# Optimization experiments

Hardware: AMD Instinct MI355X
Metric: run time of the kernel (lower is better)

## Reference

```python
import jax, jax.numpy as jnp
import numpy as np
from jax import lax

ANGRES = 5


def _conv(x, w, stride=(1, 1), pad=((1, 1), (1, 1)), dil=(1, 1)):
    return lax.conv_general_dilated(x, w, stride, pad, rhs_dilation=dil,
                                    dimension_numbers=('NCHW', 'OIHW', 'NCHW'))


def _lrelu(x):
    return jnp.where(x >= 0, x, 0.1 * x)


def _block_s(x, w):
    # SAI input: split into 5x5 grid of (sh,sw) views, conv each view, emit MacPI-interleaved layout
    B, C, H, W = x.shape
    sh, sw = H // 5, W // 5
    p = x.reshape(B, C, 5, sh, 5, sw).transpose(0, 2, 4, 1, 3, 5).reshape(B * 25, C, sh, sw)
    y = _conv(p, w).reshape(B, 5, 5, C, sh, sw)
    # (B,bi,bj,C,sh,sw) -> (B,C,sh,bi,sw,bj) -> (B,C,H,W)   [torch permute(0,3,4,1,5,2)]
    return y.transpose(0, 3, 4, 1, 5, 2).reshape(B, C, H, W)


def _block_a(x, w):
    # MacPI input: conv each 5x5 macropixel independently (zero pad at block edges)
    B, C, H, W = x.shape
    nh, nw = H // 5, W // 5
    p = x.reshape(B, C, nh, 5, nw, 5).transpose(0, 2, 4, 1, 3, 5).reshape(B * nh * nw, C, 5, 5)
    y = _conv(p, w)
    return y.reshape(B, nh, nw, C, 5, 5).transpose(0, 3, 1, 4, 2, 5).reshape(B, C, H, W)


def _epi(x, w1, w2, a):
    # EPI conv: [1,3a] kernel, stride [1,a], pad [0,a]; then 1x1 to a*C; then 1D pixel shuffle on W
    y = _lrelu(_conv(x, w1, stride=(1, a), pad=((0, 0), (a, a))))
    y = _lrelu(_conv(y, w2, pad=((0, 0), (0, 0))))
    B, aC, H, Wa = y.shape
    C = aC // a
    return y.reshape(B, a, C, H, Wa).transpose(0, 2, 3, 4, 1).reshape(B, C, H, Wa * a)


def _att_fuse(buf, alpha, gamma, beta, eps=1e-5):
    # covariance-based GLU attention over the N=4 branches
    B, NC, H, W = buf.shape
    N = 4
    C = NC // N
    x5 = buf.reshape(B, N, C, H, W)
    xr = x5.reshape(B, N, C * H * W)
    M = xr.shape[-1]
    xc = xr - jnp.mean(xr, axis=-1, keepdims=True)
    cov = jnp.einsum('bnm,bkm->bnk', xc, xc) * (alpha / (M - 1))  # [B,N,N]
    norm = cov / jnp.sqrt(jnp.mean(cov * cov, axis=(1, 2), keepdims=True) + eps)
    g = gamma * norm + beta
    att = g * jax.nn.sigmoid(g)  # GLU of duplicated halves
    out = jnp.einsum('bnk,bkm->bnm', att, xr).reshape(B, N, C, H, W) + x5
    return out.reshape(B, NC, H, W)


def _mac2sai(x, a):
    B, C, HU, WV = x.shape
    h, w = HU // a, WV // a
    return x.reshape(B, C, a, h, a, w).transpose(0, 1, 3, 5, 2, 4).reshape(B, C, h * a, w * a)


def _tsfefb(x, x1, ws, wa, we1, we2, al, ga, be, wf1, wf2, a):
    feaSpa = _lrelu(_block_s(x1, ws))
    feaAng = _lrelu(_block_a(x, wa))
    feaH = _epi(x, we1, we2, a)
    feaV = jnp.transpose(_epi(jnp.transpose(x, (0, 1, 3, 2)), we1, we2, a), (0, 1, 3, 2))
    buf = jnp.concatenate([feaSpa, feaAng, feaH, feaV], axis=1)
    out = _att_fuse(buf, al, ga, be)
    y = _lrelu(_conv(out, wf1, pad=((0, 0), (0, 0))))
    y = _conv(y, wf2, pad=((a, a), (a, a)), dil=(a, a))
    return y + x


def setup_inputs() -> dict:
    key = jax.random.key(0)
    ks = jax.random.split(key, 12)
    B, C, a, n = 4, 64, ANGRES, 4
    H = W = a * 32  # 160

    def w(k, shape):
        fan_in = float(np.prod(shape[2:]))
        return jax.random.normal(k, shape, jnp.float32) / np.float32(np.sqrt(fan_in))

    return {
        'x': jax.random.normal(ks[0], (B, C, H, W), jnp.float32),
        'x1': jax.random.normal(ks[1], (B, C, H, W), jnp.float32),
        'w_spa': w(ks[2], (n, C, C, 3, 3)),
        'w_ang': w(ks[3], (n, C, C, 3, 3)),
        'w_epi1': w(ks[4], (n, C, C, 1, 3 * a)),
        'w_epi2': w(ks[5], (n, a * C, C, 1, 1)),
        'alpha': jnp.ones((n,), jnp.float32),
        'gamma': 0.1 * jax.random.normal(ks[6], (n,), jnp.float32),
        'beta': 0.1 * jax.random.normal(ks[7], (n,), jnp.float32),
        'w_fuse1': w(ks[8], (n, C, 4 * C, 1, 1)),
        'w_fuse2': w(ks[9], (n, C, C, 3, 3)),
    }


def reference(x, x1, w_spa, w_ang, w_epi1, w_epi2, alpha, gamma, beta, w_fuse1, w_fuse2):
    a = ANGRES
    buf, buf1 = x, x1
    for i in range(w_spa.shape[0]):
        buf = _tsfefb(buf, buf1, w_spa[i], w_ang[i], w_epi1[i], w_epi2[i],
                      alpha[i], gamma[i], beta[i], w_fuse1[i], w_fuse2[i], a)
        buf1 = _mac2sai(buf, a)
    return buf
```

## Files before the change

kernel.cpp:

```cpp
#include <hip/hip_runtime.h>

__device__ __forceinline__ float lrelu(float v){ return v >= 0.f ? v : 0.1f*v; }


__global__ __launch_bounds__(256) void k_spa(const float* __restrict__ buf1, const float* __restrict__ w,
                                             float* __restrict__ out){
  const int b = blockIdx.x / 50, r2 = blockIdx.x % 50;
  const int view = r2 >> 1, half = r2 & 1;
  const int bi = view / 5, bj = view % 5;
  const int th0 = half*16;
  const int cog = blockIdx.y;
  const int tid = threadIdx.x;
  __shared__ float plane[2][18*38];
  for (int idx=tid; idx<2*18*38; idx+=256) ((float*)plane)[idx]=0.f;
  float acc[2][8];
  #pragma unroll
  for (int k=0;k<2;k++)
    #pragma unroll
    for (int c=0;c<8;c++) acc[k][c]=0.f;
  const float* src = buf1 + (size_t)b*1638400 + bi*32*160 + bj*32;
  const float* wb = w + (size_t)(cog*8)*576;
  const int sr = tid >> 3, sq = (tid & 7)*4;
  const int vr = th0 - 1 + sr;
  const bool rowok = (tid < 144) && ((unsigned)vr < 32u);
  __syncthreads();
  if (rowok)
    *(float4*)&plane[0][sr*38 + 4 + sq] = *(const float4*)(src + vr*160 + sq);
  __syncthreads();
  const int lr = tid >> 5, c = tid & 31;
  for (int ci=0; ci<64; ci++){
    float4 nx;
    const bool ld = rowok && (ci < 63);
    if (ld) nx = *(const float4*)(src + (size_t)(ci+1)*25600 + vr*160 + sq);
    const float* P = plane[ci & 1];
    float t0[9], t1[9];
    {
      const float* pp = &P[lr*38 + c + 3];
      t0[0]=pp[0];  t0[1]=pp[1];  t0[2]=pp[2];
      t0[3]=pp[38]; t0[4]=pp[39]; t0[5]=pp[40];
      t0[6]=pp[76]; t0[7]=pp[77]; t0[8]=pp[78];
      const float* qq = pp + 8*38;
      t1[0]=qq[0];  t1[1]=qq[1];  t1[2]=qq[2];
      t1[3]=qq[38]; t1[4]=qq[39]; t1[5]=qq[40];
      t1[6]=qq[76]; t1[7]=qq[77]; t1[8]=qq[78];
    }
    #pragma unroll
    for (int co=0;co<8;co++){
      const float* wp = wb + (size_t)co*576 + ci*9;
      float w0=wp[0],w1=wp[1],w2=wp[2],w3=wp[3],w4=wp[4],w5=wp[5],w6=wp[6],w7=wp[7],w8=wp[8];
      acc[0][co] += t0[0]*w0+t0[1]*w1+t0[2]*w2+t0[3]*w3+t0[4]*w4
                  + t0[5]*w5+t0[6]*w6+t0[7]*w7+t0[8]*w8;
      acc[1][co] += t1[0]*w0+t1[1]*w1+t1[2]*w2+t1[3]*w3+t1[4]*w4
                  + t1[5]*w5+t1[6]*w6+t1[7]*w7+t1[8]*w8;
    }
    if (ld) *(float4*)&plane[(ci+1)&1][sr*38 + 4 + sq] = nx;
    __syncthreads();
  }
  #pragma unroll
  for (int k=0;k<2;k++){
    int si = th0 + lr + k*8;
    int h = si*5 + bi, wq = c*5 + bj;
    #pragma unroll
    for (int co=0;co<8;co++){
      int ch = b*64 + cog*8 + co;
      out[(size_t)ch*25600 + h*160 + wq] = lrelu(acc[k][co]);
    }
  }
}

__global__ __launch_bounds__(256) void k_ang(const float* __restrict__ bufA, const float* __restrict__ w,
                                             float* __restrict__ out){
  const int b = blockIdx.x >> 5, mi = blockIdx.x & 31;
  const int cog = blockIdx.y;
  const int tid = threadIdx.x;
  __shared__ float rowp[7*172];
  for (int idx=tid; idx<7*172; idx+=256) rowp[idx]=0.f;
  float acc[4][8];
  #pragma unroll
  for (int k=0;k<4;k++)
    #pragma unroll
    for (int c=0;c<8;c++) acc[k][c]=0.f;
  int pu[4], pbase[4];
  float plm[4], prm[4];
  bool act[4];
  #pragma unroll
  for (int k=0;k<4;k++){
    int p = tid + k*256;
    act[k] = p < 800;
    int pp = act[k] ? p : 0;
    int mp = pp/25; int pos = pp - mp*25;
    int u = pos/5, v = pos - u*5;
    pu[k] = u; pbase[k] = 4 + mp*5 + v - 1;
    plm[k] = (v!=0) ? 1.f : 0.f;
    prm[k] = (v!=4) ? 1.f : 0.f;
  }
  const float* src = bufA + (size_t)b*1638400 + mi*800;
  const float* wb = w + (size_t)(cog*8)*576;
  const int sr = tid/40, sq = (tid%40)*4;
  for (int ci=0; ci<64; ci++){
    __syncthreads();
    if (tid < 200)
      *(float4*)&rowp[(1+sr)*172 + 4 + sq] = *(const float4*)(src + (size_t)ci*25600 + sr*160 + sq);
    __syncthreads();
    float t[4][9];
    #pragma unroll
    for (int k=0;k<4;k++){
      if (act[k]){
        const float* pp = &rowp[pu[k]*172 + pbase[k]];
        float lm=plm[k], rm=prm[k];
        t[k][0]=pp[0]*lm;   t[k][1]=pp[1];   t[k][2]=pp[2]*rm;
        t[k][3]=pp[172]*lm; t[k][4]=pp[173]; t[k][5]=pp[174]*rm;
        t[k][6]=pp[344]*lm; t[k][7]=pp[345]; t[k][8]=pp[346]*rm;
      } else {
        #pragma unroll
        for (int j=0;j<9;j++) t[k][j]=0.f;
      }
    }
    #pragma unroll
    for (int c=0;c<8;c++){
      const float* wp = wb + (size_t)c*576 + ci*9;
      float w0=wp[0],w1=wp[1],w2=wp[2],w3=wp[3],w4=wp[4],w5=wp[5],w6=wp[6],w7=wp[7],w8=wp[8];
      #pragma unroll
      for (int k=0;k<4;k++)
        acc[k][c] += t[k][0]*w0+t[k][1]*w1+t[k][2]*w2+t[k][3]*w3+t[k][4]*w4
                   + t[k][5]*w5+t[k][6]*w6+t[k][7]*w7+t[k][8]*w8;
    }
  }
  #pragma unroll
  for (int k=0;k<4;k++){
    if (act[k]){
      int p = tid + k*256;
      int mp = p/25; int pos = p - mp*25;
      int u = pos/5, v = pos - u*5;
      int h = mi*5 + u, wq = mp*5 + v;
      #pragma unroll
      for (int c=0;c<8;c++){
        int ch = b*64 + cog*8 + c;
        out[(size_t)ch*25600 + h*160 + wq] = lrelu(acc[k][c]);
      }
    }
  }
}

template<int VERT>
__global__ __launch_bounds__(320) void k_epi(const float* __restrict__ bufA, const float* __restrict__ we1,
                                             const float* __restrict__ we2, float* __restrict__ out){
  const int b = blockIdx.x / 160, hw = blockIdx.x % 160;
  const int tid = threadIdx.x;
  __shared__ float rowp[64*176];
  __shared__ float y1s[64*32];
  if (VERT){
    for (int idx=tid; idx<10240; idx+=320){
      int ci = idx/160, x = idx - ci*160;
      rowp[ci*176 + 8 + x] = bufA[(size_t)b*1638400 + (size_t)ci*25600 + (size_t)x*160 + hw];
    }
  } else {
    for (int ft=tid; ft<2560; ft+=320){
      int ci = ft/40, xq = (ft - ci*40)*4;
      *(float4*)&rowp[ci*176 + 8 + xq] =
        *(const float4*)(bufA + (size_t)b*1638400 + (size_t)ci*25600 + (size_t)hw*160 + xq);
    }
  }
  for (int idx=tid; idx<64*16; idx+=320){
    int ci = idx>>4, j = idx&15;
    rowp[ci*176 + (j<8 ? j : 160+j)] = 0.f;
  }
  __syncthreads();
  if (tid < 256){
    const int co = tid >> 2, wv0 = (tid & 3)*8;
    const int a0 = 2 + wv0*5;
    float acc[8];
    #pragma unroll
    for (int j=0;j<8;j++) acc[j]=0.f;
    const float* wp0 = we1 + (size_t)co*960;
    for (int ci=0; ci<64; ci++){
      float fl[52];
      const float* rp = &rowp[ci*176 + a0];
      #pragma unroll
      for (int m=0;m<26;m++) *(float2*)&fl[2*m] = *(const float2*)&rp[2*m];
      const float* wp = wp0 + ci*15;
      #pragma unroll
      for (int t=0;t<15;t++){
        float wt = wp[t];
        #pragma unroll
        for (int j=0;j<8;j++) acc[j] += fl[1 + j*5 + t]*wt;
      }
    }
    #pragma unroll
    for (int j=0;j<8;j++) y1s[co*32 + wv0 + j] = lrelu(acc[j]);
  }
  __syncthreads();
  {
    const int oc = tid, kk = oc >> 6, c = oc & 63;
    float a2[32];
    #pragma unroll
    for (int wv=0;wv<32;wv++) a2[wv]=0.f;
    const float* wp = we2 + (size_t)oc*64;
    for (int ci=0; ci<64; ci++){
      float wt = wp[ci];
      const float* yp = &y1s[ci*32];
      #pragma unroll
      for (int wv=0; wv<32; wv++) a2[wv] += yp[wv]*wt;
    }
    float* y2s = rowp;
    #pragma unroll
    for (int wv=0; wv<32; wv++) y2s[c*160 + wv*5 + kk] = lrelu(a2[wv]);
  }
  __syncthreads();
  {
    const float* y2s = rowp;
    for (int k=0;k<8;k++){
      int f = (tid + k*320)*4;
      int c = f/160, rr = f - c*160;
      *(float4*)(out + (size_t)(b*64+c)*25600 + (size_t)hw*160 + rr) = *(const float4*)&y2s[c*160+rr];
    }
  }
}

__global__ __launch_bounds__(256) void k_permV(const float* __restrict__ tmp, float* __restrict__ dst){
  const int bc = blockIdx.x;
  const int ti = blockIdx.y / 5, tj = blockIdx.y % 5;
  const int hw0 = ti*32, r0 = tj*32;
  const int lx = threadIdx.x & 31, ly = threadIdx.x >> 5;
  __shared__ float tile[32][33];
  const float* in = tmp + (size_t)bc*25600;
  float* outp = dst + (size_t)bc*25600;
  for (int yy=ly; yy<32; yy+=8)
    tile[yy][lx] = in[(size_t)(hw0+yy)*160 + r0 + lx];
  __syncthreads();
  for (int yy=ly; yy<32; yy+=8)
    outp[(size_t)(r0+yy)*160 + hw0 + lx] = tile[lx][yy];
}

__global__ __launch_bounds__(256) void k_permM(const float* __restrict__ A, float* __restrict__ dst){
  const int bc = blockIdx.x >> 5, hh = blockIdx.x & 31;
  const int tid = threadIdx.x;
  __shared__ float rows[5*160];
  const float* in = A + (size_t)bc*25600;
  if (tid < 200){
    int ai = tid/40, q = (tid - ai*40)*4;
    *(float4*)&rows[ai*160 + q] = *(const float4*)(in + (size_t)(ai*32+hh)*160 + q);
  }
  __syncthreads();
  float* outp = dst + (size_t)bc*25600 + (size_t)hh*800;
  for (int t=tid; t<800; t+=256){
    int ww = t/25, r2 = t - ww*25, ai = r2/5, aj = r2 - ai*5;
    outp[t] = rows[ai*160 + aj*32 + ww];
  }
}

__global__ __launch_bounds__(256) void k_red(const float* __restrict__ b0, const float* __restrict__ b1,
                                             const float* __restrict__ b2, const float* __restrict__ b3,
                                             float* __restrict__ part){
  const int b = blockIdx.y, blk = blockIdx.x;
  const int tid = threadIdx.x;
  const size_t off = (size_t)b*1638400 + (size_t)blk*25600;
  float s0=0,s1=0,s2=0,s3=0;
  float p00=0,p01=0,p02=0,p03=0,p11=0,p12=0,p13=0,p22=0,p23=0,p33=0;
  for (int it=0; it<25; it++){
    size_t m = off + it*1024 + tid*4;
    float4 x0 = *(const float4*)(b0+m);
    float4 x1 = *(const float4*)(b1+m);
    float4 x2 = *(const float4*)(b2+m);
    float4 x3 = *(const float4*)(b3+m);
    s0 += (x0.x+x0.y)+(x0.z+x0.w);
    s1 += (x1.x+x1.y)+(x1.z+x1.w);
    s2 += (x2.x+x2.y)+(x2.z+x2.w);
    s3 += (x3.x+x3.y)+(x3.z+x3.w);
    p00 += x0.x*x0.x+x0.y*x0.y+x0.z*x0.z+x0.w*x0.w;
    p01 += x0.x*x1.x+x0.y*x1.y+x0.z*x1.z+x0.w*x1.w;
    p02 += x0.x*x2.x+x0.y*x2.y+x0.z*x2.z+x0.w*x2.w;
    p03 += x0.x*x3.x+x0.y*x3.y+x0.z*x3.z+x0.w*x3.w;
    p11 += x1.x*x1.x+x1.y*x1.y+x1.z*x1.z+x1.w*x1.w;
    p12 += x1.x*x2.x+x1.y*x2.y+x1.z*x2.z+x1.w*x2.w;
    p13 += x1.x*x3.x+x1.y*x3.y+x1.z*x3.z+x1.w*x3.w;
    p22 += x2.x*x2.x+x2.y*x2.y+x2.z*x2.z+x2.w*x2.w;
    p23 += x2.x*x3.x+x2.y*x3.y+x2.z*x3.z+x2.w*x3.w;
    p33 += x3.x*x3.x+x3.y*x3.y+x3.z*x3.z+x3.w*x3.w;
  }
  float vals[14] = {s0,s1,s2,s3,p00,p01,p02,p03,p11,p12,p13,p22,p23,p33};
  __shared__ float red[4][14];
  int lane = tid & 63, wv = tid >> 6;
  #pragma unroll
  for (int j=0;j<14;j++){
    float v = vals[j];
    #pragma unroll
    for (int o=32;o>0;o>>=1) v += __shfl_down(v,o,64);
    if (lane==0) red[wv][j]=v;
  }
  __syncthreads();
  if (tid<14) part[((size_t)b*64+blk)*16 + tid] = red[0][tid]+red[1][tid]+red[2][tid]+red[3][tid];
}

__global__ __launch_bounds__(256) void k_attW(const float* __restrict__ part,
        const float* __restrict__ alpha, const float* __restrict__ gamma, const float* __restrict__ beta,
        int iblk, const float* __restrict__ wf1, float* __restrict__ Weff){
  const int b = blockIdx.x, tid = threadIdx.x;
  __shared__ float st[14];
  __shared__ float att[16];
  if (tid<14){
    float t=0;
    for (int blk=0;blk<64;blk++) t += part[((size_t)b*64+blk)*16 + tid];
    st[tid]=t;
  }
  __syncthreads();
  if (tid==0){
    const float M = 1638400.f;
    float s[4] = {st[0],st[1],st[2],st[3]};
    float S[4][4];
    S[0][0]=st[4];  S[0][1]=S[1][0]=st[5];  S[0][2]=S[2][0]=st[6];  S[0][3]=S[3][0]=st[7];
    S[1][1]=st[8];  S[1][2]=S[2][1]=st[9];  S[1][3]=S[3][1]=st[10];
    S[2][2]=st[11]; S[2][3]=S[3][2]=st[12]; S[3][3]=st[13];
    float al=alpha[iblk], ga=gamma[iblk], be=beta[iblk];
    float scale = al/(M-1.f);
    float cov[4][4], ss=0.f;
    for (int n=0;n<4;n++) for (int k=0;k<4;k++){
      float c = (S[n][k] - s[n]*s[k]/M)*scale;
      cov[n][k]=c; ss += c*c;
    }
    float rms = sqrtf(ss/16.f + 1e-5f);
    for (int n=0;n<4;n++) for (int k=0;k<4;k++){
      float g = ga*cov[n][k]/rms + be;
      att[n*4+k] = g/(1.f+expf(-g));
    }
  }
  __syncthreads();
  for (int idx=tid; idx<16384; idx+=256){
    int co=idx>>8, kc=idx&255, k=kc>>6, c=kc&63;
    float v = wf1[co*256+kc];
    #pragma unroll
    for (int n=0;n<4;n++) v += att[n*4+k]*wf1[co*256+n*64+c];
    Weff[(size_t)b*16384+idx] = v;
  }
}

__global__ __launch_bounds__(256) void k_fuse1(const float* b0, const float* __restrict__ b1,
                                               const float* __restrict__ b2, const float* __restrict__ b3,
                                               const float* __restrict__ Weff, float* y64){
  const int tile = blockIdx.x, b = blockIdx.y;
  const int px0 = tile*64;
  const int tid = threadIdx.x;
  const int ti = tid >> 4, tj = tid & 15;
  __shared__ float xs[64][68];
  __shared__ float wt[64][68];
  float acc[4][4];
  #pragma unroll
  for (int i=0;i<4;i++)
    #pragma unroll
    for (int j=0;j<4;j++) acc[i][j]=0.f;
  const float* bptr[4] = {b0,b1,b2,b3};
  for (int kb=0; kb<4; kb++){
    const float* xbk = bptr[kb] + (size_t)b*1638400 + px0;
    const float* wb = Weff + (size_t)b*16384 + kb*64;
    __syncthreads();
    for (int idx=tid; idx<4096; idx+=256){
      int kc=idx>>6, px=idx&63;
      xs[kc][px] = xbk[(size_t)kc*25600 + px];
    }
    for (int idx=tid; idx<4096; idx+=256){
      int co=idx>>6, k2=idx&63;
      wt[k2][co] = wb[co*256 + k2];
    }
    __syncthreads();
    for (int k2=0;k2<64;k2++){
      float4 a = *(const float4*)&wt[k2][ti*4];
      float4 v = *(const float4*)&xs[k2][tj*4];
      acc[0][0]+=a.x*v.x; acc[0][1]+=a.x*v.y; acc[0][2]+=a.x*v.z; acc[0][3]+=a.x*v.w;
      acc[1][0]+=a.y*v.x; acc[1][1]+=a.y*v.y; acc[1][2]+=a.y*v.z; acc[1][3]+=a.y*v.w;
      acc[2][0]+=a.z*v.x; acc[2][1]+=a.z*v.y; acc[2][2]+=a.z*v.z; acc[2][3]+=a.z*v.w;
      acc[3][0]+=a.w*v.x; acc[3][1]+=a.w*v.y; acc[3][2]+=a.w*v.z; acc[3][3]+=a.w*v.w;
    }
  }
  #pragma unroll
  for (int i=0;i<4;i++){
    int co = ti*4 + i;
    float4 o = make_float4(lrelu(acc[i][0]), lrelu(acc[i][1]), lrelu(acc[i][2]), lrelu(acc[i][3]));
    *(float4*)(y64 + ((size_t)(b*64+co))*25600 + px0 + tj*4) = o;
  }
}

template<int FINAL>
__global__ __launch_bounds__(256) void k_fuse2(const float* __restrict__ y64, const float* resid,
                                               const float* __restrict__ w, float* outp){
  const int b = blockIdx.x / 50, tile = blockIdx.x % 50;
  const int th0 = (tile/5)*16, tw0 = (tile%5)*32;
  const int cog = blockIdx.y;
  const int tid = threadIdx.x;
  __shared__ float plane[2][26*44];
  float acc[2][8];
  #pragma unroll
  for (int k=0;k<2;k++)
    #pragma unroll
    for (int c=0;c<8;c++) acc[k][c]=0.f;
  const float* src = y64 + (size_t)b*1638400;
  const float* wb = w + (size_t)(cog*8)*576;
  int soff[5], sdst[5];
  #pragma unroll
  for (int s=0;s<5;s++){
    int idx = tid + s*256;
    int r = idx/42, cc = idx - r*42;
    int gh = th0 + r - 5, gw = tw0 + cc - 5;
    sdst[s] = r*44 + cc;
    soff[s] = ((unsigned)gh < 160u && (unsigned)gw < 160u) ? (gh*160 + gw) : -1;
  }
  const bool s4 = (tid < 68);
  #pragma unroll
  for (int s=0;s<4;s++)
    plane[0][sdst[s]] = (soff[s] >= 0) ? src[soff[s]] : 0.f;
  if (s4) plane[0][sdst[4]] = (soff[4] >= 0) ? src[soff[4]] : 0.f;
  __syncthreads();
  const int lr = tid >> 5, c = tid & 31;
  for (int ci=0; ci<64; ci++){
    float nv[5];
    if (ci < 63){
      const float* s1 = src + (size_t)(ci+1)*25600;
      #pragma unroll
      for (int s=0;s<5;s++) nv[s] = (soff[s] >= 0) ? s1[soff[s]] : 0.f;
    }
    const float* P = plane[ci & 1];
    float t0[9], t1[9];
    {
      const float* pp = &P[lr*44 + c];
      t0[0]=pp[0];      t0[1]=pp[5];      t0[2]=pp[10];
      t0[3]=pp[220];    t0[4]=pp[225];    t0[5]=pp[230];
      t0[6]=pp[440];    t0[7]=pp[445];    t0[8]=pp[450];
      const float* qq = pp + 8*44;
      t1[0]=qq[0];      t1[1]=qq[5];      t1[2]=qq[10];
      t1[3]=qq[220];    t1[4]=qq[225];    t1[5]=qq[230];
      t1[6]=qq[440];    t1[7]=qq[445];    t1[8]=qq[450];
    }
    #pragma unroll
    for (int co=0;co<8;co++){
      const float* wp = wb + (size_t)co*576 + ci*9;
      float w0=wp[0],w1=wp[1],w2=wp[2],w3=wp[3],w4=wp[4],w5=wp[5],w6=wp[6],w7=wp[7],w8=wp[8];
      acc[0][co] += t0[0]*w0+t0[1]*w1+t0[2]*w2+t0[3]*w3+t0[4]*w4
                  + t0[5]*w5+t0[6]*w6+t0[7]*w7+t0[8]*w8;
      acc[1][co] += t1[0]*w0+t1[1]*w1+t1[2]*w2+t1[3]*w3+t1[4]*w4
                  + t1[5]*w5+t1[6]*w6+t1[7]*w7+t1[8]*w8;
    }
    if (ci < 63){
      float* Q = plane[(ci+1)&1];
      #pragma unroll
      for (int s=0;s<4;s++) Q[sdst[s]] = nv[s];
      if (s4) Q[sdst[4]] = nv[4];
    }
    __syncthreads();
  }
  #pragma unroll
  for (int k=0;k<2;k++){
    int h = th0 + lr + k*8, wq = tw0 + c;
    #pragma unroll
    for (int co=0;co<8;co++){
      int cg = cog*8 + co;
      size_t base = ((size_t)(b*64+cg)*160 + h)*160 + wq;
      outp[base] = acc[k][co] + resid[base];
    }
  }
}

extern "C" void kernel_launch(void* const* d_in, const int* in_sizes, int n_in,
                              void* d_out, int out_size, void* d_ws, size_t ws_size,
                              hipStream_t stream){
  const float* x    = (const float*)d_in[0];
  const float* x1   = (const float*)d_in[1];
  const float* wspa = (const float*)d_in[2];
  const float* wang = (const float*)d_in[3];
  const float* we1  = (const float*)d_in[4];
  const float* we2  = (const float*)d_in[5];
  const float* al   = (const float*)d_in[6];
  const float* ga   = (const float*)d_in[7];
  const float* be   = (const float*)d_in[8];
  const float* wf1  = (const float*)d_in[9];
  const float* wf2  = (const float*)d_in[10];

  char* ws = (char*)d_ws;
  const size_t SLOT = 26214400;
  float* A  = (float*)(ws);
  float* Bv = (float*)(ws +   SLOT);
  float* T1 = (float*)(ws + 2*SLOT);
  float* T2 = (float*)(ws + 3*SLOT);
  float* part = (float*)(ws + 4*SLOT);
  float* Weff = (float*)(ws + 4*SLOT + 16384);
  float* D = (float*)d_out;

  for (int i=0;i<4;i++){
    const float* Asrc  = (i==0) ? x  : (const float*)A;
    const float* B1src = (i==0) ? x1 : (const float*)Bv;
    k_epi<1><<<640,320,0,stream>>>(Asrc, we1 + (size_t)i*61440, we2 + (size_t)i*20480, T2);
    k_spa<<<dim3(200,8),256,0,stream>>>(B1src, wspa + (size_t)i*36864, T1);
    k_permV<<<dim3(256,25),256,0,stream>>>(T2, Bv);
    k_ang<<<dim3(128,8),256,0,stream>>>(Asrc, wang + (size_t)i*36864, T2);
    k_epi<0><<<640,320,0,stream>>>(Asrc, we1 + (size_t)i*61440, we2 + (size_t)i*20480, D);
    k_red<<<dim3(64,4),256,0,stream>>>(T1, T2, D, Bv, part);
    k_attW<<<4,256,0,stream>>>(part, al, ga, be, i, wf1 + (size_t)i*16384, Weff);
    k_fuse1<<<dim3(400,4),256,0,stream>>>(T1, T2, D, Bv, Weff, T1);
    if (i<3){
      k_fuse2<0><<<dim3(200,8),256,0,stream>>>(T1, Asrc, wf2 + (size_t)i*36864, A);
      k_permM<<<8192,256,0,stream>>>(A, Bv);
    } else {
      k_fuse2<1><<<dim3(200,8),256,0,stream>>>(T1, Asrc, wf2 + (size_t)i*36864, D);
    }
  }
}
```

Baseline: 3.170 ms.

## Restructure angular conv with per-thread macropixel rows and double-buffered LDS

Rewrites the macropixel 3x3 conv kernel so each thread computes a full 5-wide row of one macropixel for 4 output channels. Each block now covers two macropixel rows with 320 threads, and the grid becomes 64x16. Input planes are scattered into a split LDS layout (4-wide float4 part plus a separate 5th column) and double-buffered, with the next channel prefetched into registers during compute. This removes one barrier per channel and lets adjacent outputs share loaded values, replacing the 9 masked loads per output. The cost is fewer output channels per block, so weights are reloaded more often, and the scattered LDS stores may cause bank conflicts.

```diff
diff --git a/kernel.cpp b/kernel.cpp
--- a/kernel.cpp
+++ b/kernel.cpp
@@ -68,77 +68,104 @@
   }
 }
 
-__global__ __launch_bounds__(256) void k_ang(const float* __restrict__ bufA, const float* __restrict__ w,
+__global__ __launch_bounds__(320) void k_ang(const float* __restrict__ bufA, const float* __restrict__ w,
                                              float* __restrict__ out){
-  const int b = blockIdx.x >> 5, mi = blockIdx.x & 31;
+  const int b = blockIdx.x >> 4, mip = blockIdx.x & 15;
   const int cog = blockIdx.y;
   const int tid = threadIdx.x;
-  __shared__ float rowp[7*172];
-  for (int idx=tid; idx<7*172; idx+=256) rowp[idx]=0.f;
-  float acc[4][8];
-  #pragma unroll
-  for (int k=0;k<4;k++)
-    #pragma unroll
-    for (int c=0;c<8;c++) acc[k][c]=0.f;
-  int pu[4], pbase[4];
-  float plm[4], prm[4];
-  bool act[4];
-  #pragma unroll
-  for (int k=0;k<4;k++){
-    int p = tid + k*256;
-    act[k] = p < 800;
-    int pp = act[k] ? p : 0;
-    int mp = pp/25; int pos = pp - mp*25;
-    int u = pos/5, v = pos - u*5;
-    pu[k] = u; pbase[k] = 4 + mp*5 + v - 1;
-    plm[k] = (v!=0) ? 1.f : 0.f;
-    prm[k] = (v!=4) ? 1.f : 0.f;
-  }
-  const float* src = bufA + (size_t)b*1638400 + mi*800;
-  const float* wb = w + (size_t)(cog*8)*576;
-  const int sr = tid/40, sq = (tid%40)*4;
+  __shared__ float lds[2][2240];
+  for (int i=tid; i<2*2240; i+=320) ((float*)lds)[i] = 0.f;
+
+  const int u = tid >> 6, mi_l = (tid >> 5) & 1, mp = tid & 31;
+  int offm[3], offa[3];
+  #pragma unroll
+  for (int du=0; du<3; du++){
+    offm[du] = mi_l*896 + (u+du)*128 + mp*4;
+    offa[du] = 1792 + mi_l*224 + (u+du)*32 + mp;
+  }
+  const bool st1 = tid < 80;
+  int sdst0[4], sdst1[4];
+  const int rr0 = tid/40,       q0 = tid%40;
+  const int rr1 = (tid+320)/40, q1 = (tid+320)%40;
+  #pragma unroll
+  for (int j=0;j<4;j++){
+    int g = q0*4+j, mpw = g/5, vw = g - mpw*5;
+    int miw = rr0/5, uw = rr0 - miw*5;
+    sdst0[j] = (vw<4) ? (miw*896 + (1+uw)*128 + mpw*4 + vw)
+                      : (1792 + miw*224 + (1+uw)*32 + mpw);
+    g = q1*4+j; mpw = g/5; vw = g - mpw*5;
+    miw = rr1/5; uw = rr1 - miw*5;
+    sdst1[j] = (vw<4) ? (miw*896 + (1+uw)*128 + mpw*4 + vw)
+                      : (1792 + miw*224 + (1+uw)*32 + mpw);
+  }
+  const float* src = bufA + (size_t)b*1638400 + (size_t)(mip*10)*160;
+  const float* wb = w + (size_t)(cog*4)*576;
+
+  float acc[4][5];
+  #pragma unroll
+  for (int co=0;co<4;co++)
+    #pragma unroll
+    for (int v=0;v<5;v++) acc[co][v]=0.f;
+
+  __syncthreads();
+  {
+    float4 x0 = *(const float4*)(src + rr0*160 + q0*4);
+    lds[0][sdst0[0]]=x0.x; lds[0][sdst0[1]]=x0.y; lds[0][sdst0[2]]=x0.z; lds[0][sdst0[3]]=x0.w;
+    if (st1){
+      float4 x1 = *(const float4*)(src + rr1*160 + q1*4);
+      lds[0][sdst1[0]]=x1.x; lds[0][sdst1[1]]=x1.y; lds[0][sdst1[2]]=x1.z; lds[0][sdst1[3]]=x1.w;
+    }
+  }
+  __syncthreads();
   for (int ci=0; ci<64; ci++){
+    float4 n0, n1;
+    if (ci < 63){
+      n0 = *(const float4*)(src + (size_t)(ci+1)*25600 + rr0*160 + q0*4);
+      if (st1) n1 = *(const float4*)(src + (size_t)(ci+1)*25600 + rr1*160 + q1*4);
+    }
+    const float* P = lds[ci & 1];
+    float c[3][5];
+    #pragma unroll
+    for (int du=0;du<3;du++){
+      float4 m = *(const float4*)&P[offm[du]];
+      c[du][0]=m.x; c[du][1]=m.y; c[du][2]=m.z; c[du][3]=m.w;
+      c[du][4]=P[offa[du]];
+    }
+    #pragma unroll
+    for (int co=0;co<4;co++){
+      const float* wp = wb + (size_t)co*576 + ci*9;
+      float w0=wp[0],w1=wp[1],w2=wp[2],w3=wp[3],w4=wp[4],w5=wp[5],w6=wp[6],w7=wp[7],w8=wp[8];
+      acc[co][0] += c[0][0]*w1 + c[0][1]*w2
+                  + c[1][0]*w4 + c[1][1]*w5
+                  + c[2][0]*w7 + c[2][1]*w8;
+      acc[co][1] += c[0][0]*w0 + c[0][1]*w1 + c[0][2]*w2
+                  + c[1][0]*w3 + c[1][1]*w4 + c[1][2]*w5
+                  + c[2][0]*w6 + c[2][1]*w7 + c[2][2]*w8;
+      acc[co][2] += c[0][1]*w0 + c[0][2]*w1 + c[0][3]*w2
+                  + c[1][1]*w3 + c[1][2]*w4 + c[1][3]*w5
+                  + c[2][1]*w6 + c[2][2]*w7 + c[2][3]*w8;
+      acc[co][3] += c[0][2]*w0 + c[0][3]*w1 + c[0][4]*w2
+                  + c[1][2]*w3 + c[1][3]*w4 + c[1][4]*w5
+                  + c[2][2]*w6 + c[2][3]*w7 + c[2][4]*w8;
+      acc[co][4] += c[0][3]*w0 + c[0][4]*w1
+                  + c[1][3]*w3 + c[1][4]*w4
+                  + c[2][3]*w6 + c[2][4]*w7;
+    }
+    if (ci < 63){
+      float* Q = lds[(ci+1)&1];
+      Q[sdst0[0]]=n0.x; Q[sdst0[1]]=n0.y; Q[sdst0[2]]=n0.z; Q[sdst0[3]]=n0.w;
+      if (st1){ Q[sdst1[0]]=n1.x; Q[sdst1[1]]=n1.y; Q[sdst1[2]]=n1.z; Q[sdst1[3]]=n1.w; }
+    }
     __syncthreads();
-    if (tid < 200)
-      *(float4*)&rowp[(1+sr)*172 + 4 + sq] = *(const float4*)(src + (size_t)ci*25600 + sr*160 + sq);
-    __syncthreads();
-    float t[4][9];
-    #pragma unroll
-    for (int k=0;k<4;k++){
-      if (act[k]){
-        const float* pp = &rowp[pu[k]*172 + pbase[k]];
-        float lm=plm[k], rm=prm[k];
-        t[k][0]=pp[0]*lm;   t[k][1]=pp[1];   t[k][2]=pp[2]*rm;
-        t[k][3]=pp[172]*lm; t[k][4]=pp[173]; t[k][5]=pp[174]*rm;
-        t[k][6]=pp[344]*lm; t[k][7]=pp[345]; t[k][8]=pp[346]*rm;
-      } else {
-        #pragma unroll
-        for (int j=0;j<9;j++) t[k][j]=0.f;
-      }
-    }
-    #pragma unroll
-    for (int c=0;c<8;c++){
-      const float* wp = wb + (size_t)c*576 + ci*9;
-      float w0=wp[0],w1=wp[1],w2=wp[2],w3=wp[3],w4=wp[4],w5=wp[5],w6=wp[6],w7=wp[7],w8=wp[8];
-      #pragma unroll
-      for (int k=0;k<4;k++)
-        acc[k][c] += t[k][0]*w0+t[k][1]*w1+t[k][2]*w2+t[k][3]*w3+t[k][4]*w4
-                   + t[k][5]*w5+t[k][6]*w6+t[k][7]*w7+t[k][8]*w8;
-    }
-  }
-  #pragma unroll
-  for (int k=0;k<4;k++){
-    if (act[k]){
-      int p = tid + k*256;
-      int mp = p/25; int pos = p - mp*25;
-      int u = pos/5, v = pos - u*5;
-      int h = mi*5 + u, wq = mp*5 + v;
-      #pragma unroll
-      for (int c=0;c<8;c++){
-        int ch = b*64 + cog*8 + c;
-        out[(size_t)ch*25600 + h*160 + wq] = lrelu(acc[k][c]);
-      }
-    }
+  }
+  const int h = (mip*2 + mi_l)*5 + u;
+  const int wc0 = mp*5;
+  #pragma unroll
+  for (int co=0;co<4;co++){
+    int ch = b*64 + cog*4 + co;
+    float* op = out + (size_t)ch*25600 + (size_t)h*160 + wc0;
+    op[0]=lrelu(acc[co][0]); op[1]=lrelu(acc[co][1]); op[2]=lrelu(acc[co][2]);
+    op[3]=lrelu(acc[co][3]); op[4]=lrelu(acc[co][4]);
   }
 }
 
@@ -489,7 +516,7 @@
     k_epi<1><<<640,320,0,stream>>>(Asrc, we1 + (size_t)i*61440, we2 + (size_t)i*20480, T2);
     k_spa<<<dim3(200,8),256,0,stream>>>(B1src, wspa + (size_t)i*36864, T1);
     k_permV<<<dim3(256,25),256,0,stream>>>(T2, Bv);
-    k_ang<<<dim3(128,8),256,0,stream>>>(Asrc, wang + (size_t)i*36864, T2);
+    k_ang<<<dim3(64,16),320,0,stream>>>(Asrc, wang + (size_t)i*36864, T2);
     k_epi<0><<<640,320,0,stream>>>(Asrc, we1 + (size_t)i*61440, we2 + (size_t)i*20480, D);
     k_red<<<dim3(64,4),256,0,stream>>>(T1, T2, D, Bv, part);
     k_attW<<<4,256,0,stream>>>(part, al, ga, be, i, wf1 + (size_t)i*16384, Weff);
```

New measurement: 3.108 ms. -2.0%, faster.
